# Performance work log

Hardware: AMD Instinct MI355X
Metric: run time of the kernel (lower is better)

Reference implementation:

```python
import jax, jax.numpy as jnp
import numpy as np

N = 1_000_000          # number of query points
POINT_DIMS = 2         # (x, y) coordinates
NUM_EMB = 6572         # number of video frames
EMB_DIM = 32
HIDDEN = 128


def setup_inputs() -> dict:
    key = jax.random.key(0)
    ks = jax.random.split(key, 10)
    x = jax.random.uniform(ks[0], (N, POINT_DIMS), dtype=jnp.float32)
    # fractional frame index in [0, NUM_EMB - 1)
    embeddings = jax.random.uniform(ks[1], (N,), dtype=jnp.float32) * (NUM_EMB - 1)
    em_table = jax.random.normal(ks[2], (NUM_EMB, EMB_DIM), dtype=jnp.float32) * 0.1
    in0 = POINT_DIMS + EMB_DIM
    W0 = jax.random.normal(ks[3], (in0, HIDDEN), dtype=jnp.float32) / np.sqrt(in0)
    b0 = jax.random.normal(ks[4], (HIDDEN,), dtype=jnp.float32) * 0.01
    W1 = jax.random.normal(ks[5], (HIDDEN, HIDDEN), dtype=jnp.float32) / np.sqrt(HIDDEN)
    b1 = jax.random.normal(ks[6], (HIDDEN,), dtype=jnp.float32) * 0.01
    W2 = jax.random.normal(ks[7], (HIDDEN, 1), dtype=jnp.float32) / np.sqrt(HIDDEN)
    b2 = jax.random.normal(ks[8], (1,), dtype=jnp.float32) * 0.01
    return {"x": x, "embeddings": embeddings, "em_table": em_table,
            "W0": W0, "b0": b0, "W1": W1, "b1": b1, "W2": W2, "b2": b2}


def reference(x, embeddings, em_table, W0, b0, W1, b1, W2, b2):
    num_emb = em_table.shape[0]
    em1 = embeddings.astype(jnp.int32)                       # floor (inputs >= 0)
    em2 = jnp.minimum(em1 + 1, num_emb - 1)                  # clamp(em1+1, max=E-1)
    res = (embeddings - em1.astype(jnp.float32))[:, None]    # [N, 1]
    e1 = em_table[em1]                                       # [N, 32] gather
    e2 = em_table[em2]                                       # [N, 32] gather
    em = e1 + (e2 - e1) * res                                # lerp
    h = jnp.concatenate((x, em), axis=1) @ W0 + b0           # [N, 128]
    h = jnp.clip(h, 0.0, 1.0)
    h = jnp.clip(h @ W1 + b1, 0.0, 1.0)
    out = jax.nn.sigmoid(h @ W2 + b2)                        # [N, 1]
    return out
```

## Files before the change

kernel.cpp:

```cpp
#include <hip/hip_runtime.h>
#include <hip/hip_bf16.h>


using bf16x8 = __attribute__((ext_vector_type(8))) short;
using f32x4  = __attribute__((ext_vector_type(4))) float;

#define NPTS    1000000
#define NUMEMB  6572
#define HID     128
#define M_IT    64
#define A0S     72
#define H0S     136
#define TILES   (NPTS / M_IT)
#define NBLOCKS 768

__device__ __forceinline__ unsigned short bf16r(float f) {
    unsigned u;
    __builtin_memcpy(&u, &f, 4);
    u = (u + 0x7fffu + ((u >> 16) & 1u)) >> 16;
    return (unsigned short)u;
}
__device__ __forceinline__ unsigned pk2(float a, float b) {
    float2 f2; f2.x = a; f2.y = b;
    __hip_bfloat162 h = __float22bfloat162_rn(f2);
    unsigned u;
    __builtin_memcpy(&u, &h, 4);
    return u;
}
__device__ __forceinline__ float clamp01(float x) {
    return __builtin_amdgcn_fmed3f(x, 0.f, 1.f);
}

__global__ __launch_bounds__(256, 3)
void mlp_fused(const float* __restrict__ x,
               const float* __restrict__ emb,
               const float* __restrict__ em_table,
               const float* __restrict__ W0, const float* __restrict__ b0,
               const float* __restrict__ W1, const float* __restrict__ b1,
               const float* __restrict__ W2, const float* __restrict__ b2,
               float* __restrict__ out)
{
    __shared__ __align__(16) unsigned short A0[M_IT * A0S];
    __shared__ __align__(16) unsigned short H0[M_IT * H0S];
    __shared__ __align__(16) float PART[16][M_IT];

    const int tid  = threadIdx.x;
    const int lane = tid & 63;
    const int nq   = tid >> 6;
    const int q    = lane >> 4;
    const int cl   = lane & 15;
    const int p    = tid >> 2;
    const int s    = tid & 3;

    for (int i = tid; i < M_IT * A0S; i += 256) A0[i] = 0;

    const int hcol = nq * 32 + (cl >> 2) * 8 + (cl & 3);
    bf16x8 w0t[2][2];
    for (int hb = 0; hb < 2; ++hb)
        for (int kt = 0; kt < 2; ++kt) {
            const int col = hcol + hb * 4;
            bf16x8 v;
            #pragma unroll
            for (int e = 0; e < 8; ++e) {
                const int k = kt * 32 + q * 8 + e;
                float val = 0.f;
                if (k < 32)       val = W0[(2 + k) * HID + col];
                else if (k == 32) val = W0[0 * HID + col];
                else if (k == 33) val = W0[1 * HID + col];
                v[e] = (short)bf16r(val);
            }
            w0t[hb][kt] = v;
        }

    bf16x8 w1r[2][4];
    for (int hb = 0; hb < 2; ++hb)
        for (int kk = 0; kk < 4; ++kk) {
            const int kt  = (nq + kk) & 3;
            const int col = hcol + hb * 4;
            bf16x8 v;
            #pragma unroll
            for (int e = 0; e < 8; ++e) {
                const int k = kt * 32 + q * 8 + e;
                v[e] = (short)bf16r(W1[k * HID + col]);
            }
            w1r[hb][kk] = v;
        }

    f32x4 b0q[2], b1q[2], w2q[2];
    for (int hb = 0; hb < 2; ++hb)
        for (int r = 0; r < 4; ++r) {
            const int h = nq * 32 + q * 8 + hb * 4 + r;
            b0q[hb][r] = b0[h];
            b1q[hb][r] = b1[h];
            w2q[hb][r] = W2[h];
        }
    const float bias2 = b2[0];

    int t = blockIdx.x;
    float  feA;
    float2 xvA = {0.f, 0.f};
    {
        const int gp = t * M_IT + p;
        feA = emb[gp];
        if (s == 0) xvA = *(const float2*)(x + 2 * gp);
    }

    __syncthreads();

    for (; t < TILES; t += gridDim.x) {
        const int base = t * M_IT;

        {
            const int e1 = (int)feA;
            const int e2 = (e1 + 1 < NUMEMB) ? e1 + 1 : NUMEMB - 1;
            const float r = feA - (float)e1;
            const float4* p1 = (const float4*)(em_table + e1 * 32 + s * 8);
            const float4* p2 = (const float4*)(em_table + e2 * 32 + s * 8);
            const float4 a0v = p1[0], a1v = p1[1];
            const float4 c0v = p2[0], c1v = p2[1];
            uint4 d;
            d.x = pk2(a0v.x + (c0v.x - a0v.x) * r, a0v.y + (c0v.y - a0v.y) * r);
            d.y = pk2(a0v.z + (c0v.z - a0v.z) * r, a0v.w + (c0v.w - a0v.w) * r);
            d.z = pk2(a1v.x + (c1v.x - a1v.x) * r, a1v.y + (c1v.y - a1v.y) * r);
            d.w = pk2(a1v.z + (c1v.z - a1v.z) * r, a1v.w + (c1v.w - a1v.w) * r);
            *(uint4*)&A0[p * A0S + s * 8] = d;
            if (s == 0) *(unsigned*)&A0[p * A0S + 32] = pk2(xvA.x, xvA.y);
        }
        __syncthreads();

        f32x4 acc[4][2];
        #pragma unroll
        for (int pb = 0; pb < 4; ++pb)
            #pragma unroll
            for (int hb = 0; hb < 2; ++hb)
                acc[pb][hb] = b0q[hb];
        #pragma unroll
        for (int pb = 0; pb < 4; ++pb) {
            #pragma unroll
            for (int kt = 0; kt < 2; ++kt) {
                bf16x8 bfrag = *(const bf16x8*)
                    &A0[(pb * 16 + cl) * A0S + kt * 32 + q * 8];
                #pragma unroll
                for (int hb = 0; hb < 2; ++hb)
                    acc[pb][hb] = __builtin_amdgcn_mfma_f32_16x16x32_bf16(
                        w0t[hb][kt], bfrag, acc[pb][hb], 0, 0, 0);
            }
        }

        {
            int t1 = t + gridDim.x; if (t1 >= TILES) t1 = t;
            const int gp = t1 * M_IT + p;
            feA = emb[gp];
            if (s == 0) xvA = *(const float2*)(x + 2 * gp);
        }

        uint4 own[4];
        #pragma unroll
        for (int pb = 0; pb < 4; ++pb) {
            const f32x4 v0 = acc[pb][0], v1 = acc[pb][1];
            uint4 w;
            w.x = pk2(clamp01(v0[0]), clamp01(v0[1]));
            w.y = pk2(clamp01(v0[2]), clamp01(v0[3]));
            w.z = pk2(clamp01(v1[0]), clamp01(v1[1]));
            w.w = pk2(clamp01(v1[2]), clamp01(v1[3]));
            own[pb] = w;
            *(uint4*)&H0[(pb * 16 + cl) * H0S + nq * 32 + q * 8] = w;
        }
        __syncthreads();

        #pragma unroll
        for (int pb = 0; pb < 4; ++pb)
            #pragma unroll
            for (int hb = 0; hb < 2; ++hb)
                acc[pb][hb] = b1q[hb];
        #pragma unroll
        for (int pb = 0; pb < 4; ++pb) {
            bf16x8 bfrag;
            __builtin_memcpy(&bfrag, &own[pb], 16);
            #pragma unroll
            for (int hb = 0; hb < 2; ++hb)
                acc[pb][hb] = __builtin_amdgcn_mfma_f32_16x16x32_bf16(
                    w1r[hb][0], bfrag, acc[pb][hb], 0, 0, 0);
        }
        #pragma unroll
        for (int kk = 1; kk < 4; ++kk) {
            const int kcol = (((nq + kk) & 3) << 5) + q * 8;
            #pragma unroll
            for (int pb = 0; pb < 4; ++pb) {
                bf16x8 bfrag = *(const bf16x8*)
                    &H0[(pb * 16 + cl) * H0S + kcol];
                #pragma unroll
                for (int hb = 0; hb < 2; ++hb)
                    acc[pb][hb] = __builtin_amdgcn_mfma_f32_16x16x32_bf16(
                        w1r[hb][kk], bfrag, acc[pb][hb], 0, 0, 0);
            }
        }

        #pragma unroll
        for (int pb = 0; pb < 4; ++pb) {
            float sum = 0.f;
            #pragma unroll
            for (int hb = 0; hb < 2; ++hb) {
                const f32x4 v = acc[pb][hb];
                sum += clamp01(v[0]) * w2q[hb][0];
                sum += clamp01(v[1]) * w2q[hb][1];
                sum += clamp01(v[2]) * w2q[hb][2];
                sum += clamp01(v[3]) * w2q[hb][3];
            }
            PART[nq * 4 + q][pb * 16 + cl] = sum;
        }
        __syncthreads();

        if (tid < 64) {
            float z = bias2;
            #pragma unroll
            for (int i = 0; i < 16; ++i) z += PART[i][tid];
            out[base + tid] = 1.f / (1.f + __expf(-z));
        }
    }
}

extern "C" void kernel_launch(void* const* d_in, const int* in_sizes, int n_in,
                              void* d_out, int out_size, void* d_ws, size_t ws_size,
                              hipStream_t stream) {
    const float* x   = (const float*)d_in[0];
    const float* emb = (const float*)d_in[1];
    const float* emt = (const float*)d_in[2];
    const float* W0  = (const float*)d_in[3];
    const float* b0  = (const float*)d_in[4];
    const float* W1  = (const float*)d_in[5];
    const float* b1  = (const float*)d_in[6];
    const float* W2  = (const float*)d_in[7];
    const float* b2  = (const float*)d_in[8];
    mlp_fused<<<NBLOCKS, 256, 0, stream>>>(x, emb, emt, W0, b0, W1, b1, W2, b2,
                                           (float*)d_out);
}
```

Baseline: 126.5 us.

## Double-buffer embedding tile and prefetch next tile's gather during compute

Splits the A0 staging tile into two LDS buffers and moves the embedding-table gather and lerp for the next tile into the current iteration. The gather is issued after the first MFMA layer and written after the H0 store, which removes one __syncthreads per tile and hides gather latency behind compute. Input prefetch now looks two tiles ahead. PART is padded to 65 columns to reduce LDS bank conflicts. The cost is more LDS per block and extra live registers, which may reduce occupancy under launch_bounds(256,3).

```diff
diff --git a/kernel.cpp b/kernel.cpp
--- a/kernel.cpp
+++ b/kernel.cpp
@@ -40,9 +40,9 @@
                const float* __restrict__ W2, const float* __restrict__ b2,
                float* __restrict__ out)
 {
-    __shared__ __align__(16) unsigned short A0[M_IT * A0S];
+    __shared__ __align__(16) unsigned short A0[2 * M_IT * A0S];
     __shared__ __align__(16) unsigned short H0[M_IT * H0S];
-    __shared__ __align__(16) float PART[16][M_IT];
+    __shared__ __align__(16) float PART[16][65];
 
     const int tid  = threadIdx.x;
     const int lane = tid & 63;
@@ -52,7 +52,7 @@
     const int p    = tid >> 2;
     const int s    = tid & 3;
 
-    for (int i = tid; i < M_IT * A0S; i += 256) A0[i] = 0;
+    for (int i = tid; i < 2 * M_IT * A0S; i += 256) A0[i] = 0;
 
     const int hcol = nq * 32 + (cl >> 2) * 8 + (cl & 3);
     bf16x8 w0t[2][2];
@@ -97,36 +97,41 @@
     const float bias2 = b2[0];
 
     int t = blockIdx.x;
-    float  feA;
-    float2 xvA = {0.f, 0.f};
+    int cur = 0;
     {
         const int gp = t * M_IT + p;
-        feA = emb[gp];
-        if (s == 0) xvA = *(const float2*)(x + 2 * gp);
+        const float fe = emb[gp];
+        float2 xv = {0.f, 0.f};
+        if (s == 0) xv = *(const float2*)(x + 2 * gp);
+        const int e1 = (int)fe;
+        const int e2 = (e1 + 1 < NUMEMB) ? e1 + 1 : NUMEMB - 1;
+        const float r = fe - (float)e1;
+        const float4* p1 = (const float4*)(em_table + e1 * 32 + s * 8);
+        const float4* p2 = (const float4*)(em_table + e2 * 32 + s * 8);
+        const float4 g0 = p1[0], g1 = p1[1], g2 = p2[0], g3 = p2[1];
+        uint4 d;
+        d.x = pk2(g0.x + (g2.x - g0.x) * r, g0.y + (g2.y - g0.y) * r);
+        d.y = pk2(g0.z + (g2.z - g0.z) * r, g0.w + (g2.w - g0.w) * r);
+        d.z = pk2(g1.x + (g3.x - g1.x) * r, g1.y + (g3.y - g1.y) * r);
+        d.w = pk2(g1.z + (g3.z - g1.z) * r, g1.w + (g3.w - g1.w) * r);
+        *(uint4*)&A0[p * A0S + s * 8] = d;
+        if (s == 0) *(unsigned*)&A0[p * A0S + 32] = pk2(xv.x, xv.y);
     }
+    float  feB;
+    float2 xvB = {0.f, 0.f};
+    {
+        int t1 = t + gridDim.x; if (t1 >= TILES) t1 = t;
+        const int gp = t1 * M_IT + p;
+        feB = emb[gp];
+        if (s == 0) xvB = *(const float2*)(x + 2 * gp);
+    }
 
     __syncthreads();
 
-    for (; t < TILES; t += gridDim.x) {
+    for (; t < TILES; t += gridDim.x, cur ^= 1) {
         const int base = t * M_IT;
-
-        {
-            const int e1 = (int)feA;
-            const int e2 = (e1 + 1 < NUMEMB) ? e1 + 1 : NUMEMB - 1;
-            const float r = feA - (float)e1;
-            const float4* p1 = (const float4*)(em_table + e1 * 32 + s * 8);
-            const float4* p2 = (const float4*)(em_table + e2 * 32 + s * 8);
-            const float4 a0v = p1[0], a1v = p1[1];
-            const float4 c0v = p2[0], c1v = p2[1];
-            uint4 d;
-            d.x = pk2(a0v.x + (c0v.x - a0v.x) * r, a0v.y + (c0v.y - a0v.y) * r);
-            d.y = pk2(a0v.z + (c0v.z - a0v.z) * r, a0v.w + (c0v.w - a0v.w) * r);
-            d.z = pk2(a1v.x + (c1v.x - a1v.x) * r, a1v.y + (c1v.y - a1v.y) * r);
-            d.w = pk2(a1v.z + (c1v.z - a1v.z) * r, a1v.w + (c1v.w - a1v.w) * r);
-            *(uint4*)&A0[p * A0S + s * 8] = d;
-            if (s == 0) *(unsigned*)&A0[p * A0S + 32] = pk2(xvA.x, xvA.y);
-        }
-        __syncthreads();
+        const unsigned short* A0c = A0 + cur * (M_IT * A0S);
+        unsigned short*       A0n = A0 + (cur ^ 1) * (M_IT * A0S);
 
         f32x4 acc[4][2];
         #pragma unroll
@@ -139,7 +144,7 @@
             #pragma unroll
             for (int kt = 0; kt < 2; ++kt) {
                 bf16x8 bfrag = *(const bf16x8*)
-                    &A0[(pb * 16 + cl) * A0S + kt * 32 + q * 8];
+                    &A0c[(pb * 16 + cl) * A0S + kt * 32 + q * 8];
                 #pragma unroll
                 for (int hb = 0; hb < 2; ++hb)
                     acc[pb][hb] = __builtin_amdgcn_mfma_f32_16x16x32_bf16(
@@ -147,12 +152,11 @@
             }
         }
 
-        {
-            int t1 = t + gridDim.x; if (t1 >= TILES) t1 = t;
-            const int gp = t1 * M_IT + p;
-            feA = emb[gp];
-            if (s == 0) xvA = *(const float2*)(x + 2 * gp);
-        }
+        const int ge1 = (int)feB;
+        const int ge2 = (ge1 + 1 < NUMEMB) ? ge1 + 1 : NUMEMB - 1;
+        const float4* gp1 = (const float4*)(em_table + ge1 * 32 + s * 8);
+        const float4* gp2 = (const float4*)(em_table + ge2 * 32 + s * 8);
+        const float4 g0 = gp1[0], g1 = gp1[1], g2 = gp2[0], g3 = gp2[1];
 
         uint4 own[4];
         #pragma unroll
@@ -165,6 +169,23 @@
             w.w = pk2(clamp01(v1[2]), clamp01(v1[3]));
             own[pb] = w;
             *(uint4*)&H0[(pb * 16 + cl) * H0S + nq * 32 + q * 8] = w;
+        }
+
+        {
+            const float r = feB - (float)ge1;
+            uint4 d;
+            d.x = pk2(g0.x + (g2.x - g0.x) * r, g0.y + (g2.y - g0.y) * r);
+            d.y = pk2(g0.z + (g2.z - g0.z) * r, g0.w + (g2.w - g0.w) * r);
+            d.z = pk2(g1.x + (g3.x - g1.x) * r, g1.y + (g3.y - g1.y) * r);
+            d.w = pk2(g1.z + (g3.z - g1.z) * r, g1.w + (g3.w - g1.w) * r);
+            *(uint4*)&A0n[p * A0S + s * 8] = d;
+            if (s == 0) *(unsigned*)&A0n[p * A0S + 32] = pk2(xvB.x, xvB.y);
+        }
+        {
+            int t2 = t + 2 * (int)gridDim.x; if (t2 >= TILES) t2 = t;
+            const int gp = t2 * M_IT + p;
+            feB = emb[gp];
+            if (s == 0) xvB = *(const float2*)(x + 2 * gp);
         }
         __syncthreads();
 
```

After: 126.5 us. Within noise of the previous version (+0.0%).
